# Kernel tuning notes

Measured on AMD Instinct MI355X. Metric: run time of the kernel, lower is better.

Reference implementation:

```python
import jax, jax.numpy as jnp
import numpy as np

ALPHA = 0.95
TH_MIN = 0.4
TH_MAX = 1.5
LN_EPS = 1e-5
NORM_EPS = 1e-12


def setup_inputs() -> dict:
    key = jax.random.key(0)
    ks = jax.random.split(key, 8)
    B, L, H, V = 64, 2048, 128, 32000
    s = 1.0 / np.sqrt(H)
    return {
        "seq": jax.random.randint(ks[0], (B, L), 0, V),
        "embed": jax.random.normal(ks[1], (V, H), jnp.float32),
        "w1": jax.random.normal(ks[2], (H, 2 * H), jnp.float32) * s,
        "b1": jnp.zeros((2 * H,), jnp.float32),
        "w2": jax.random.normal(ks[3], (2 * H, H), jnp.float32) * (1.0 / np.sqrt(2 * H)),
        "b2": jnp.zeros((H,), jnp.float32),
        "ln_g": jnp.ones((H,), jnp.float32),
        "ln_b": jnp.zeros((H,), jnp.float32),
        "kp_w": jax.random.normal(ks[4], (H, H), jnp.float32) * s,
        "rp_w": jax.random.normal(ks[5], (H, H), jnp.float32) * s,
        "rp_b": jnp.zeros((H,), jnp.float32),
        "out_w": jax.random.normal(ks[6], (H, V), jnp.float32) * s,
        "out_b": jnp.zeros((V,), jnp.float32),
    }


def reference(seq, embed, w1, b1, w2, b2, ln_g, ln_b, kp_w, rp_w, rp_b, out_w, out_b):
    # Embedding + residual FFN + LayerNorm
    h = embed[seq]  # [B,L,H]
    x = h + (jnp.maximum(h @ w1 + b1, 0.0) @ w2 + b2)
    mu = jnp.mean(x, axis=-1, keepdims=True)
    var = jnp.mean(jnp.square(x - mu), axis=-1, keepdims=True)
    hn = (x - mu) * jax.lax.rsqrt(var + LN_EPS) * ln_g + ln_b
    B, L, H = hn.shape

    keys = hn @ kp_w  # [B,L,H] all projected keys (kp has no bias)
    ks_t = jnp.swapaxes(keys[:, :-1, :], 0, 1)  # [L-1,B,H] time-major for scan
    t_idx = jnp.arange(L - 1, dtype=hn.dtype)
    thresh = TH_MIN + (TH_MAX - TH_MIN) * (1.0 - t_idx / max(L - 1, 1))  # [L-1]

    def step(M, inputs):
        k, th = inputs  # k: [B,H], th: scalar
        kn = k / jnp.maximum(jnp.linalg.norm(k, axis=-1, keepdims=True), NORM_EPS)
        vp = jnp.einsum('bij,bj->bi', M, kn)  # predicted value
        err = k - vp
        fire = (jnp.linalg.norm(err, axis=-1) >= th * jnp.linalg.norm(k, axis=-1)).astype(M.dtype)
        delta = fire[:, None, None] * (err[:, :, None] * kn[:, None, :])  # gated outer product
        return M + (1.0 - ALPHA) * delta, None

    M0 = jnp.zeros((B, H, H), hn.dtype)
    M, _ = jax.lax.scan(step, M0, (ks_t, thresh))

    q = keys[:, -1, :]
    read = jnp.einsum('bij,bj->bi', M, q)
    return (read @ rp_w + rp_b) @ out_w + out_b
```

## Files before the change

kernel.cpp:

```cpp
#include <hip/hip_runtime.h>

#define HD 128
#define LD 2048
#define BD 64
#define VD 32000
#define NSTEP 2047

#define C_ALPHA  0.05f
#define C_THMIN  0.4f
#define C_THSPAN 1.1f
#define C_NEPS   1e-12f
#define C_LNEPS  1e-5f

#define HSP 132
#define W1P 68
#define W2P 132
#define ATP 68
#define TOK0 896
#define TBLK 9

extern "C" __global__ __launch_bounds__(256, 1)
void k_tokens(const int* __restrict__ seq, const float* __restrict__ embed,
              const float* __restrict__ w1, const float* __restrict__ b1,
              const float* __restrict__ w2, const float* __restrict__ b2,
              const float* __restrict__ lng, const float* __restrict__ lnb,
              const float* __restrict__ kp, float* __restrict__ keys)
{
  extern __shared__ float sm[];
  float* hs = sm;
  float* wt = sm + 128*HSP;
  float* at = wt + 128*W1P;
  const int tid = threadIdx.x;
  const int bb  = blockIdx.x / TBLK;
  const int rel = blockIdx.x % TBLK;
  const long long tokBase = (long long)bb * LD + TOK0 + rel * 128;

  for (int u = tid; u < 128*32; u += 256) {
    const int tok = u >> 5, seg = u & 31;
    const int s = seq[tokBase + tok];
    *(float4*)(hs + tok*HSP + seg*4) =
        *(const float4*)(embed + (long long)s*HD + seg*4);
  }
  __syncthreads();

  const int tg = tid >> 4;
  const int ig = tid & 15;

  float xacc[8][8] = {};

  for (int jt = 0; jt < 4; ++jt) {
    for (int u = tid; u < 128*16; u += 256) {
      const int i = u >> 4, q = u & 15;
      *(float4*)(wt + i*W1P + q*4) =
          *(const float4*)(w1 + (long long)i*256 + jt*64 + q*4);
    }
    __syncthreads();
    {
      float aa[8][4];
      float b1v[4];
      #pragma unroll
      for (int c = 0; c < 4; ++c) b1v[c] = b1[jt*64 + ig*4 + c];
      #pragma unroll
      for (int r = 0; r < 8; ++r)
        #pragma unroll
        for (int c = 0; c < 4; ++c) aa[r][c] = b1v[c];
      #pragma unroll 4
      for (int i4 = 0; i4 < 32; ++i4) {
        float wc[4][4];
        #pragma unroll
        for (int d = 0; d < 4; ++d) {
          float4 u = *(const float4*)(wt + (i4*4 + d)*W1P + ig*4);
          wc[d][0] = u.x; wc[d][1] = u.y; wc[d][2] = u.z; wc[d][3] = u.w;
        }
        #pragma unroll
        for (int r = 0; r < 8; ++r) {
          float4 hv = *(const float4*)(hs + (tg + 16*r)*HSP + i4*4);
          #pragma unroll
          for (int c = 0; c < 4; ++c) {
            aa[r][c] = fmaf(hv.x, wc[0][c], aa[r][c]);
            aa[r][c] = fmaf(hv.y, wc[1][c], aa[r][c]);
            aa[r][c] = fmaf(hv.z, wc[2][c], aa[r][c]);
            aa[r][c] = fmaf(hv.w, wc[3][c], aa[r][c]);
          }
        }
      }
      #pragma unroll
      for (int r = 0; r < 8; ++r) {
        float4 o;
        o.x = fmaxf(aa[r][0], 0.0f); o.y = fmaxf(aa[r][1], 0.0f);
        o.z = fmaxf(aa[r][2], 0.0f); o.w = fmaxf(aa[r][3], 0.0f);
        *(float4*)(at + (tg + 16*r)*ATP + ig*4) = o;
      }
    }
    __syncthreads();
    for (int u = tid; u < 64*32; u += 256) {
      const int k = u >> 5, q = u & 31;
      *(float4*)(wt + k*W2P + q*4) =
          *(const float4*)(w2 + (long long)(jt*64 + k)*128 + q*4);
    }
    __syncthreads();
    #pragma unroll 2
    for (int k4 = 0; k4 < 16; ++k4) {
      float wr[4][8];
      #pragma unroll
      for (int d = 0; d < 4; ++d) {
        float4 u0 = *(const float4*)(wt + (k4*4 + d)*W2P + ig*8);
        float4 u1 = *(const float4*)(wt + (k4*4 + d)*W2P + ig*8 + 4);
        wr[d][0]=u0.x; wr[d][1]=u0.y; wr[d][2]=u0.z; wr[d][3]=u0.w;
        wr[d][4]=u1.x; wr[d][5]=u1.y; wr[d][6]=u1.z; wr[d][7]=u1.w;
      }
      #pragma unroll
      for (int r = 0; r < 8; ++r) {
        float4 av = *(const float4*)(at + (tg + 16*r)*ATP + k4*4);
        #pragma unroll
        for (int cc = 0; cc < 8; ++cc) {
          xacc[r][cc] = fmaf(av.x, wr[0][cc], xacc[r][cc]);
          xacc[r][cc] = fmaf(av.y, wr[1][cc], xacc[r][cc]);
          xacc[r][cc] = fmaf(av.z, wr[2][cc], xacc[r][cc]);
          xacc[r][cc] = fmaf(av.w, wr[3][cc], xacc[r][cc]);
        }
      }
    }
    __syncthreads();
  }

  {
    float b2v[8], gv[8], bv[8];
    #pragma unroll
    for (int cc = 0; cc < 8; ++cc) {
      b2v[cc] = b2[ig*8 + cc]; gv[cc] = lng[ig*8 + cc]; bv[cc] = lnb[ig*8 + cc];
    }
    #pragma unroll
    for (int r = 0; r < 8; ++r) {
      const int row = (tg + 16*r)*HSP + ig*8;
      float4 h0 = *(const float4*)(hs + row);
      float4 h1 = *(const float4*)(hs + row + 4);
      float xr[8];
      xr[0] = h0.x + (xacc[r][0] + b2v[0]);
      xr[1] = h0.y + (xacc[r][1] + b2v[1]);
      xr[2] = h0.z + (xacc[r][2] + b2v[2]);
      xr[3] = h0.w + (xacc[r][3] + b2v[3]);
      xr[4] = h1.x + (xacc[r][4] + b2v[4]);
      xr[5] = h1.y + (xacc[r][5] + b2v[5]);
      xr[6] = h1.z + (xacc[r][6] + b2v[6]);
      xr[7] = h1.w + (xacc[r][7] + b2v[7]);
      float s = xr[0]+xr[1]+xr[2]+xr[3]+xr[4]+xr[5]+xr[6]+xr[7];
      s += __shfl_xor(s, 1, 16); s += __shfl_xor(s, 2, 16);
      s += __shfl_xor(s, 4, 16); s += __shfl_xor(s, 8, 16);
      const float mu = s * 0.0078125f;
      float vs = 0.0f;
      #pragma unroll
      for (int cc = 0; cc < 8; ++cc) { float d = xr[cc]-mu; vs = fmaf(d, d, vs); }
      vs += __shfl_xor(vs, 1, 16); vs += __shfl_xor(vs, 2, 16);
      vs += __shfl_xor(vs, 4, 16); vs += __shfl_xor(vs, 8, 16);
      const float rstd = 1.0f / sqrtf(vs * 0.0078125f + C_LNEPS);
      float4 o0, o1;
      o0.x = (xr[0]-mu)*rstd*gv[0] + bv[0];
      o0.y = (xr[1]-mu)*rstd*gv[1] + bv[1];
      o0.z = (xr[2]-mu)*rstd*gv[2] + bv[2];
      o0.w = (xr[3]-mu)*rstd*gv[3] + bv[3];
      o1.x = (xr[4]-mu)*rstd*gv[4] + bv[4];
      o1.y = (xr[5]-mu)*rstd*gv[5] + bv[5];
      o1.z = (xr[6]-mu)*rstd*gv[6] + bv[6];
      o1.w = (xr[7]-mu)*rstd*gv[7] + bv[7];
      *(float4*)(hs + row) = o0;
      *(float4*)(hs + row + 4) = o1;
    }
  }
  __syncthreads();

  {
    float ky[8][8] = {};
    for (int kt = 0; kt < 2; ++kt) {
      for (int u = tid; u < 64*32; u += 256) {
        const int k = u >> 5, q = u & 31;
        *(float4*)(wt + k*W2P + q*4) =
            *(const float4*)(kp + (long long)(kt*64 + k)*128 + q*4);
      }
      __syncthreads();
      #pragma unroll 2
      for (int k4 = 0; k4 < 16; ++k4) {
        float wr[4][8];
        #pragma unroll
        for (int d = 0; d < 4; ++d) {
          float4 u0 = *(const float4*)(wt + (k4*4 + d)*W2P + ig*8);
          float4 u1 = *(const float4*)(wt + (k4*4 + d)*W2P + ig*8 + 4);
          wr[d][0]=u0.x; wr[d][1]=u0.y; wr[d][2]=u0.z; wr[d][3]=u0.w;
          wr[d][4]=u1.x; wr[d][5]=u1.y; wr[d][6]=u1.z; wr[d][7]=u1.w;
        }
        #pragma unroll
        for (int r = 0; r < 8; ++r) {
          float4 hv = *(const float4*)(hs + (tg + 16*r)*HSP + kt*64 + k4*4);
          #pragma unroll
          for (int cc = 0; cc < 8; ++cc) {
            ky[r][cc] = fmaf(hv.x, wr[0][cc], ky[r][cc]);
            ky[r][cc] = fmaf(hv.y, wr[1][cc], ky[r][cc]);
            ky[r][cc] = fmaf(hv.z, wr[2][cc], ky[r][cc]);
            ky[r][cc] = fmaf(hv.w, wr[3][cc], ky[r][cc]);
          }
        }
      }
      __syncthreads();
    }
    #pragma unroll
    for (int r = 0; r < 8; ++r) {
      const long long g = tokBase + tg + 16*r;
      float4 o0, o1;
      o0.x = ky[r][0]; o0.y = ky[r][1]; o0.z = ky[r][2]; o0.w = ky[r][3];
      o1.x = ky[r][4]; o1.y = ky[r][5]; o1.z = ky[r][6]; o1.w = ky[r][7];
      *(float4*)(keys + g*HD + ig*8) = o0;
      *(float4*)(keys + g*HD + ig*8 + 4) = o1;
    }
  }
}

#define C0 29
#define MSP 132
#define GPW 36
#define NT 768

#define INVB(buf,tok) Gxl[(tok)*GPW + 32 + (buf)]
#define TN2B(buf,tok) Gxl[(tok)*GPW + 34 + (buf)]

__device__ __forceinline__ float dpp_add_b1(float x){int y=__builtin_amdgcn_update_dpp(0,__float_as_int(x),0xB1,0xf,0xf,true);return x+__int_as_float(y);}
__device__ __forceinline__ float dpp_add_4e(float x){int y=__builtin_amdgcn_update_dpp(0,__float_as_int(x),0x4E,0xf,0xf,true);return x+__int_as_float(y);}
__device__ __forceinline__ float dpp_add_hm(float x){int y=__builtin_amdgcn_update_dpp(0,__float_as_int(x),0x141,0xf,0xf,true);return x+__int_as_float(y);}
__device__ __forceinline__ float dpp_add_mr(float x){int y=__builtin_amdgcn_update_dpp(0,__float_as_int(x),0x140,0xf,0xf,true);return x+__int_as_float(y);}
__device__ __forceinline__ float dpp_add_b15(float x){int y=__builtin_amdgcn_update_dpp(0,__float_as_int(x),0x142,0xf,0xf,true);return x+__int_as_float(y);}
__device__ __forceinline__ float dpp_add_b31(float x){int y=__builtin_amdgcn_update_dpp(0,__float_as_int(x),0x143,0xf,0xf,true);return x+__int_as_float(y);}

__device__ __forceinline__ void gram_half(const float* bufS, const float* bufT,
                                          float* dst, int half, int lane)
{
  const int sq = lane & 7, tq = lane >> 3;
  float ga[4][2] = {};
  for (int j4 = 0; j4 < 32; ++j4) {
    const int col = ((j4 + lane) & 31) * 4;
    float4 sv[4], tv[2];
    #pragma unroll
    for (int r = 0; r < 4; ++r)
      sv[r] = *(const float4*)(bufS + (sq + 8*r)*128 + col);
    #pragma unroll
    for (int q = 0; q < 2; ++q)
      tv[q] = *(const float4*)(bufT + (half*16 + tq*2 + q)*128 + col);
    #pragma unroll
    for (int r = 0; r < 4; ++r)
      #pragma unroll
      for (int q = 0; q < 2; ++q) {
        ga[r][q] = fmaf(sv[r].x, tv[q].x, ga[r][q]);
        ga[r][q] = fmaf(sv[r].y, tv[q].y, ga[r][q]);
        ga[r][q] = fmaf(sv[r].z, tv[q].z, ga[r][q]);
        ga[r][q] = fmaf(sv[r].w, tv[q].w, ga[r][q]);
      }
  }
  #pragma unroll
  for (int r = 0; r < 4; ++r)
    #pragma unroll
    for (int q = 0; q < 2; ++q)
      dst[(sq + 8*r)*GPW + half*16 + tq*2 + q] = ga[r][q];
}

extern "C" __global__ __launch_bounds__(768)
void k_scan(const float* __restrict__ keys, float* __restrict__ Mg)
{
  extern __shared__ float sm[];
  float* Msh  = sm;
  float* kbuf = Msh + 128*MSP;
  float* PW   = kbuf + 3*4096;
  float* Gb   = PW + 2*4096;
  float* Gxl  = Gb + 2*32*GPW;

  const int tid  = threadIdx.x;
  const int lane = tid & 63;
  const int w    = tid >> 6;
  const int b    = blockIdx.x;
  const float* kb = keys + (long long)b * LD * HD;

  for (int u = tid; u < 128*MSP; u += NT) Msh[u] = 0.0f;
  for (int u = tid; u < 4096; u += NT) PW[(C0&1)*4096 + u] = 0.0f;
  {
    const int b30 = C0 % 3;
    for (int u = tid; u < 1024; u += NT)
      *(float4*)(kbuf + b30*4096 + u*4) =
          *(const float4*)(kb + (long long)(C0*32)*HD + u*4);
  }
  __syncthreads();
  {
    const float* kc = kbuf + (C0%3)*4096;
    for (int u = tid; u < 1024; u += NT) {
      const int s = u >> 5, t = u & 31;
      float a = 0.0f;
      for (int j4 = 0; j4 < 32; ++j4) {
        const int col = ((j4 + tid) & 31) * 4;
        float4 sv = *(const float4*)(kc + s*128 + col);
        float4 tv = *(const float4*)(kc + t*128 + col);
        a = fmaf(sv.x,tv.x,a); a = fmaf(sv.y,tv.y,a);
        a = fmaf(sv.z,tv.z,a); a = fmaf(sv.w,tv.w,a);
      }
      Gb[(C0&1)*32*GPW + s*GPW + t] = a;
    }
  }
  if (tid < 256) {
    const int tok = tid >> 3, pp = tid & 7;
    const float* kc = kbuf + (C0%3)*4096;
    float ss = 0.0f;
    #pragma unroll
    for (int q = 0; q < 4; ++q) {
      float4 v = *(const float4*)(kc + tok*128 + pp*16 + q*4);
      ss = fmaf(v.x,v.x,ss); ss = fmaf(v.y,v.y,ss);
      ss = fmaf(v.z,v.z,ss); ss = fmaf(v.w,v.w,ss);
    }
    ss += __shfl_xor(ss,1,8); ss += __shfl_xor(ss,2,8); ss += __shfl_xor(ss,4,8);
    if (pp == 0) {
      const float n = sqrtf(ss);
      INVB(C0&1, tok) = 1.0f / fmaxf(n, C_NEPS);
      const float th = C_THMIN + C_THSPAN * (1.0f - (float)(C0*32 + tok) / 2047.0f);
      const float tn = th * n;
      TN2B(C0&1, tok) = tn * tn;
    }
  }
  __syncthreads();

  for (int c = C0; c <= 64; ++c) {
    const int cur = c & 1, nxt = cur ^ 1;
    const int b3c = c % 3;
    const int b3n = (c + 1) % 3;
    const int b3p = (c + 2) % 3;
    const int t0 = c * 32;

    if (w < 8) {
      if (c > C0) {
        const int it = tid >> 5;
        const int jt = tid & 31;
        const int i0 = it*8, j0 = jt*4;
        const float* Wp  = PW + nxt*4096;
        const float* kfp = kbuf + b3p*4096;
        float acc[8][4] = {};
        for (int s = 0; s < 32; ++s) {
          const float4 wa = *(const float4*)(Wp + s*128 + i0);
          const float4 wb = *(const float4*)(Wp + s*128 + i0 + 4);
          const float4 k4 = *(const float4*)(kfp + s*128 + j0);
          float wv[8] = {wa.x,wa.y,wa.z,wa.w,wb.x,wb.y,wb.z,wb.w};
          float kv[4] = {k4.x,k4.y,k4.z,k4.w};
          #pragma unroll
          for (int a = 0; a < 8; ++a)
            #pragma unroll
            for (int q = 0; q < 4; ++q)
              acc[a][q] = fmaf(wv[a], kv[q], acc[a][q]);
        }
        #pragma unroll
        for (int a = 0; a < 8; ++a) {
          float* mp = Msh + (i0 + a)*MSP + j0;
          float4 m = *(float4*)mp;
          m.x = fmaf(C_ALPHA, acc[a][0], m.x);
          m.y = fmaf(C_ALPHA, acc[a][1], m.y);
          m.z = fmaf(C_ALPHA, acc[a][2], m.z);
          m.w = fmaf(C_ALPHA, acc[a][3], m.w);
          *(float4*)mp = m;
        }
      }
    } else {
      const int t2id = tid - 512;
      float4 kvl[4];
      if (c < 63) {
        #pragma unroll
        for (int q = 0; q < 4; ++q)
          kvl[q] = *(const float4*)(kb + (long long)(t0 + 32)*HD + (t2id + 256*q)*4);
      }
      if (c > C0 && c <= 63) {
        const int tt = t2id >> 5;
        const int i0 = (t2id & 31) * 4;
        const int tb4 = tt*4;
        const float* Wp = PW + nxt*4096;
        float fac[4][4] = {};
        for (int s = 0; s < 32; ++s) {
          const float4 gx = *(const float4*)(Gxl + s*GPW + tb4);
          const float4 wp = *(const float4*)(Wp + s*128 + i0);
          float gv[4] = {gx.x,gx.y,gx.z,gx.w};
          float pv[4] = {wp.x,wp.y,wp.z,wp.w};
          #pragma unroll
          for (int a = 0; a < 4; ++a)
            #pragma unroll
            for (int q = 0; q < 4; ++q)
              fac[a][q] = fmaf(gv[a], pv[q], fac[a][q]);
        }
        float* Pp = PW + cur*4096;
        #pragma unroll
        for (int a = 0; a < 4; ++a) {
          float* pp = Pp + (tb4 + a)*128 + i0;
          float4 p = *(float4*)pp;
          p.x = fmaf(C_ALPHA, fac[a][0], p.x);
          p.y = fmaf(C_ALPHA, fac[a][1], p.y);
          p.z = fmaf(C_ALPHA, fac[a][2], p.z);
          p.w = fmaf(C_ALPHA, fac[a][3], p.w);
          *(float4*)pp = p;
        }
      }
      if (c < 63) {
        #pragma unroll
        for (int q = 0; q < 4; ++q)
          *(float4*)(kbuf + b3n*4096 + (t2id + 256*q)*4) = kvl[q];
      }
    }
    __syncthreads();
    if (c == 64) break;

    if (w == 0) {
      float* Pc = PW + cur*4096;
      const float* kfc = kbuf + b3c*4096;
      const float* Gc  = Gb + cur*32*GPW;
      const int l2 = lane*2;
      float2 acc[16];
      #pragma unroll
      for (int u = 0; u < 16; ++u) { acc[u].x = 0.0f; acc[u].y = 0.0f; }
      #pragma unroll
      for (int t = 0; t < 16; ++t) {
        const float2 p2 = *(const float2*)(Pc + t*128 + l2);
        const float2 k2 = *(const float2*)(kfc + t*128 + l2);
        const float it = INVB(cur, t);
        const float vx = it * fmaf(C_ALPHA, acc[t].x, p2.x);
        const float vy = it * fmaf(C_ALPHA, acc[t].y, p2.y);
        const float ex = k2.x - vx;
        const float ey = k2.y - vy;
        float e2 = fmaf(ex, ex, ey*ey);
        e2 = dpp_add_b1(e2); e2 = dpp_add_4e(e2);
        e2 = dpp_add_hm(e2); e2 = dpp_add_mr(e2);
        e2 = dpp_add_b15(e2); e2 = dpp_add_b31(e2);
        const float en2 = __int_as_float(__builtin_amdgcn_readlane(__float_as_int(e2), 63));
        const bool fire = (en2 >= TN2B(cur, t));
        const float wx = fire ? ex * it : 0.0f;
        const float wy = fire ? ey * it : 0.0f;
        float2 w2v; w2v.x = wx; w2v.y = wy;
        *(float2*)(Pc + t*128 + l2) = w2v;
        const float* gr = Gc + t*GPW;
        #pragma unroll
        for (int u4 = (t+1) & ~3; u4 < 16; u4 += 4) {
          const float4 g = *(const float4*)(gr + u4);
          acc[u4+0].x = fmaf(wx, g.x, acc[u4+0].x); acc[u4+0].y = fmaf(wy, g.x, acc[u4+0].y);
          acc[u4+1].x = fmaf(wx, g.y, acc[u4+1].x); acc[u4+1].y = fmaf(wy, g.y, acc[u4+1].y);
          acc[u4+2].x = fmaf(wx, g.z, acc[u4+2].x); acc[u4+2].y = fmaf(wy, g.z, acc[u4+2].y);
          acc[u4+3].x = fmaf(wx, g.w, acc[u4+3].x); acc[u4+3].y = fmaf(wy, g.w, acc[u4+3].y);
        }
      }
      #pragma unroll
      for (int u = 0; u < 16; ++u) { acc[u].x = 0.0f; acc[u].y = 0.0f; }
      #pragma unroll
      for (int s = 0; s < 16; ++s) {
        const float2 ws = *(const float2*)(Pc + s*128 + l2);
        const float* gs = Gc + s*GPW + 16;
        #pragma unroll
        for (int u4 = 0; u4 < 16; u4 += 4) {
          const float4 g = *(const float4*)(gs + u4);
          acc[u4+0].x = fmaf(ws.x, g.x, acc[u4+0].x); acc[u4+0].y = fmaf(ws.y, g.x, acc[u4+0].y);
          acc[u4+1].x = fmaf(ws.x, g.y, acc[u4+1].x); acc[u4+1].y = fmaf(ws.y, g.y, acc[u4+1].y);
          acc[u4+2].x = fmaf(ws.x, g.z, acc[u4+2].x); acc[u4+2].y = fmaf(ws.y, g.z, acc[u4+2].y);
          acc[u4+3].x = fmaf(ws.x, g.w, acc[u4+3].x); acc[u4+3].y = fmaf(ws.y, g.w, acc[u4+3].y);
        }
      }
      #pragma unroll
      for (int t = 16; t < 32; ++t) {
        const int tt = t - 16;
        const float2 p2 = *(const float2*)(Pc + t*128 + l2);
        const float2 k2 = *(const float2*)(kfc + t*128 + l2);
        const float it = INVB(cur, t);
        const float vx = it * fmaf(C_ALPHA, acc[tt].x, p2.x);
        const float vy = it * fmaf(C_ALPHA, acc[tt].y, p2.y);
        const float ex = k2.x - vx;
        const float ey = k2.y - vy;
        float e2 = fmaf(ex, ex, ey*ey);
        e2 = dpp_add_b1(e2); e2 = dpp_add_4e(e2);
        e2 = dpp_add_hm(e2); e2 = dpp_add_mr(e2);
        e2 = dpp_add_b15(e2); e2 = dpp_add_b31(e2);
        const float en2 = __int_as_float(__builtin_amdgcn_readlane(__float_as_int(e2), 63));
        const bool fire = (en2 >= TN2B(cur, t)) && (t0 + t < NSTEP);
        const float wx = fire ? ex * it : 0.0f;
        const float wy = fire ? ey * it : 0.0f;
        float2 w2v; w2v.x = wx; w2v.y = wy;
        *(float2*)(Pc + t*128 + l2) = w2v;
        const float* gr = Gc + t*GPW + 16;
        #pragma unroll
        for (int u4 = (tt+1) & ~3; u4 < 16; u4 += 4) {
          const float4 g = *(const float4*)(gr + u4);
          acc[u4+0].x = fmaf(wx, g.x, acc[u4+0].x); acc[u4+0].y = fmaf(wy, g.x, acc[u4+0].y);
          acc[u4+1].x = fmaf(wx, g.y, acc[u4+1].x); acc[u4+1].y = fmaf(wy, g.y, acc[u4+1].y);
          acc[u4+2].x = fmaf(wx, g.z, acc[u4+2].x); acc[u4+2].y = fmaf(wy, g.z, acc[u4+2].y);
          acc[u4+3].x = fmaf(wx, g.w, acc[u4+3].x); acc[u4+3].y = fmaf(wy, g.w, acc[u4+3].y);
        }
      }
    } else if (c < 63) {
      int p;
      switch (w) {
        case 4:  p = 0; break;  case 8:  p = 1; break;
        case 1:  p = 2; break;  case 5:  p = 3; break;  case 9:  p = 4; break;
        case 2:  p = 5; break;  case 6:  p = 6; break;  case 10: p = 7; break;
        default: p = -1;
      }
      if (p >= 0) {
        const float* kfn = kbuf + b3n*4096;
        const int tb4 = p*4;
        const int ib = lane & 31, ih = lane >> 5;
        float pa[4][2] = {};
        for (int j4 = 0; j4 < 32; ++j4) {
          float4 kv[4], mv[2];
          #pragma unroll
          for (int ss = 0; ss < 4; ++ss)
            kv[ss] = *(const float4*)(kfn + (tb4+ss)*128 + j4*4);
          #pragma unroll
          for (int r = 0; r < 2; ++r)
            mv[r] = *(const float4*)(Msh + (ib + 32*(ih + 2*r))*MSP + j4*4);
          #pragma unroll
          for (int ss = 0; ss < 4; ++ss)
            #pragma unroll
            for (int r = 0; r < 2; ++r) {
              pa[ss][r] = fmaf(kv[ss].x, mv[r].x, pa[ss][r]);
              pa[ss][r] = fmaf(kv[ss].y, mv[r].y, pa[ss][r]);
              pa[ss][r] = fmaf(kv[ss].z, mv[r].z, pa[ss][r]);
              pa[ss][r] = fmaf(kv[ss].w, mv[r].w, pa[ss][r]);
            }
        }
        float* Pp = PW + nxt*4096;
        #pragma unroll
        for (int ss = 0; ss < 4; ++ss)
          #pragma unroll
          for (int r = 0; r < 2; ++r)
            Pp[(tb4+ss)*128 + ib + 32*(ih + 2*r)] = pa[ss][r];
        if (w == 4) {
          const float* kn = kbuf + b3n*4096;
          const int tok = lane >> 1, hh = lane & 1;
          float ss2 = 0.0f;
          #pragma unroll
          for (int q = 0; q < 16; ++q) {
            const int cq = (q + lane) & 15;
            float4 v = *(const float4*)(kn + tok*128 + hh*64 + cq*4);
            ss2 = fmaf(v.x,v.x,ss2); ss2 = fmaf(v.y,v.y,ss2);
            ss2 = fmaf(v.z,v.z,ss2); ss2 = fmaf(v.w,v.w,ss2);
          }
          ss2 += __shfl_xor(ss2, 1);
          if (hh == 0) {
            const float n = sqrtf(ss2);
            INVB(nxt, tok) = 1.0f / fmaxf(n, C_NEPS);
            const float th = C_THMIN + C_THSPAN * (1.0f - (float)(t0 + 32 + tok) / 2047.0f);
            const float tn = th * n;
            TN2B(nxt, tok) = tn * tn;
          }
        }
      } else if (w == 3) {
        gram_half(kbuf + b3n*4096, kbuf + b3n*4096, Gb + nxt*32*GPW, 0, lane);
      } else if (w == 7) {
        gram_half(kbuf + b3n*4096, kbuf + b3n*4096, Gb + nxt*32*GPW, 1, lane);
      } else {
        gram_half(kbuf + b3c*4096, kbuf + b3n*4096, Gxl, 0, lane);
        gram_half(kbuf + b3c*4096, kbuf + b3n*4096, Gxl, 1, lane);
      }
    }
    __syncthreads();
  }

  for (int u = tid; u < 4096; u += NT) {
    const int i = u >> 5, q = u & 31;
    *(float4*)(Mg + (long long)b*16384 + i*128 + q*4) =
        *(const float4*)(Msh + i*MSP + q*4);
  }
}

extern "C" __global__ __launch_bounds__(128, 1)
void k_read(const float* __restrict__ keys, const float* __restrict__ Mg,
            const float* __restrict__ rpw, const float* __restrict__ rpb,
            float* __restrict__ rr)
{
  __shared__ float qv[128];
  __shared__ float rd[128];
  const int b = blockIdx.x, tid = threadIdx.x;
  qv[tid] = keys[((long long)b*LD + (LD-1))*HD + tid];
  __syncthreads();
  float acc = 0.0f;
  const float* Mrow = Mg + (long long)b*16384 + (long long)tid*128;
  for (int j4 = 0; j4 < 32; ++j4) {
    float4 m = *(const float4*)(Mrow + j4*4);
    acc = fmaf(m.x, qv[j4*4+0], acc);
    acc = fmaf(m.y, qv[j4*4+1], acc);
    acc = fmaf(m.z, qv[j4*4+2], acc);
    acc = fmaf(m.w, qv[j4*4+3], acc);
  }
  rd[tid] = acc;
  __syncthreads();
  float a2 = rpb[tid];
  for (int k = 0; k < 128; ++k) a2 = fmaf(rd[k], rpw[k*128 + tid], a2);
  rr[b*128 + tid] = a2;
}

extern "C" __global__ __launch_bounds__(256, 1)
void k_out(const float* __restrict__ rr, const float* __restrict__ outw,
           const float* __restrict__ outb, float* __restrict__ out)
{
  __shared__ float rl[64*128];
  const int tid = threadIdx.x;
  for (int u = tid; u < 8192; u += 256) rl[u] = rr[u];
  __syncthreads();
  const int v = blockIdx.x*128 + (tid & 127);
  const int bg = tid >> 7;
  const float ob = outb[v];
  float acc[32];
  #pragma unroll
  for (int bb = 0; bb < 32; ++bb) acc[bb] = 0.0f;
  for (int h = 0; h < 128; ++h) {
    const float wv = outw[(long long)h*VD + v];
    #pragma unroll
    for (int bb = 0; bb < 32; ++bb)
      acc[bb] = fmaf(rl[(bg*32 + bb)*128 + h], wv, acc[bb]);
  }
  #pragma unroll
  for (int bb = 0; bb < 32; ++bb)
    out[(long long)(bg*32 + bb)*VD + v] = acc[bb] + ob;
}

extern "C" void kernel_launch(void* const* d_in, const int* in_sizes, int n_in,
                              void* d_out, int out_size, void* d_ws, size_t ws_size,
                              hipStream_t stream)
{
  const int*   seq   = (const int*)d_in[0];
  const float* embed = (const float*)d_in[1];
  const float* w1    = (const float*)d_in[2];
  const float* b1    = (const float*)d_in[3];
  const float* w2    = (const float*)d_in[4];
  const float* b2    = (const float*)d_in[5];
  const float* ln_g  = (const float*)d_in[6];
  const float* ln_b  = (const float*)d_in[7];
  const float* kp_w  = (const float*)d_in[8];
  const float* rp_w  = (const float*)d_in[9];
  const float* rp_b  = (const float*)d_in[10];
  const float* out_w = (const float*)d_in[11];
  const float* out_b = (const float*)d_in[12];
  float* out = (float*)d_out;

  char* ws = (char*)d_ws;
  float* keys = (float*)ws;
  float* Mg   = (float*)(ws + 67108864);
  float* rr   = (float*)(ws + 67108864 + 4194304);

  hipLaunchKernelGGL(k_tokens, dim3(64*TBLK), dim3(256), 137216, stream,
                     seq, embed, w1, b1, w2, b2, ln_g, ln_b, kp_w, keys);
  hipLaunchKernelGGL(k_scan, dim3(64), dim3(768), 163328, stream, keys, Mg);
  hipLaunchKernelGGL(k_read, dim3(64), dim3(128), 0, stream, keys, Mg, rp_w, rp_b, rr);
  hipLaunchKernelGGL(k_out, dim3(250), dim3(256), 0, stream, rr, out_w, out_b, out);
}
```

Before: 780.2 us.

## Shrink scan block to 512 threads and redistribute per-chunk work across 8 waves

Reduces the k_scan workgroup from 12 to 8 wavefronts and rebalances the chunk work among them. The M update and the P-factor update now run on all 8 waves instead of separate wave groups. The projection, Gram and norm tasks are reassigned: waves 1-4 each handle 8 tokens, waves 5-7 handle quarter-Gram pieces, and wave 7 also computes the norms. Fewer waves should cut barrier cost and per-wave overhead, but with only 64 blocks there is less parallelism to hide LDS latency, and each wave carries more serial work.

```diff
diff --git a/kernel.cpp b/kernel.cpp
--- a/kernel.cpp
+++ b/kernel.cpp
@@ -217,7 +217,7 @@
 #define C0 29
 #define MSP 132
 #define GPW 36
-#define NT 768
+#define NT 512
 
 #define INVB(buf,tok) Gxl[(tok)*GPW + 32 + (buf)]
 #define TN2B(buf,tok) Gxl[(tok)*GPW + 34 + (buf)]
@@ -229,38 +229,28 @@
 __device__ __forceinline__ float dpp_add_b15(float x){int y=__builtin_amdgcn_update_dpp(0,__float_as_int(x),0x142,0xf,0xf,true);return x+__int_as_float(y);}
 __device__ __forceinline__ float dpp_add_b31(float x){int y=__builtin_amdgcn_update_dpp(0,__float_as_int(x),0x143,0xf,0xf,true);return x+__int_as_float(y);}
 
-__device__ __forceinline__ void gram_half(const float* bufS, const float* bufT,
-                                          float* dst, int half, int lane)
+__device__ __forceinline__ void gram_q(const float* bufS, const float* bufT,
+                                       float* dst, int q, int lane)
 {
   const int sq = lane & 7, tq = lane >> 3;
-  float ga[4][2] = {};
+  const int tcol = q*8 + tq;
+  float ga[4] = {};
   for (int j4 = 0; j4 < 32; ++j4) {
     const int col = ((j4 + lane) & 31) * 4;
-    float4 sv[4], tv[2];
+    const float4 tv = *(const float4*)(bufT + tcol*128 + col);
     #pragma unroll
-    for (int r = 0; r < 4; ++r)
-      sv[r] = *(const float4*)(bufS + (sq + 8*r)*128 + col);
-    #pragma unroll
-    for (int q = 0; q < 2; ++q)
-      tv[q] = *(const float4*)(bufT + (half*16 + tq*2 + q)*128 + col);
-    #pragma unroll
-    for (int r = 0; r < 4; ++r)
-      #pragma unroll
-      for (int q = 0; q < 2; ++q) {
-        ga[r][q] = fmaf(sv[r].x, tv[q].x, ga[r][q]);
-        ga[r][q] = fmaf(sv[r].y, tv[q].y, ga[r][q]);
-        ga[r][q] = fmaf(sv[r].z, tv[q].z, ga[r][q]);
-        ga[r][q] = fmaf(sv[r].w, tv[q].w, ga[r][q]);
-      }
+    for (int r = 0; r < 4; ++r) {
+      const float4 sv = *(const float4*)(bufS + (sq + 8*r)*128 + col);
+      ga[r] = fmaf(sv.x, tv.x, ga[r]); ga[r] = fmaf(sv.y, tv.y, ga[r]);
+      ga[r] = fmaf(sv.z, tv.z, ga[r]); ga[r] = fmaf(sv.w, tv.w, ga[r]);
+    }
   }
   #pragma unroll
   for (int r = 0; r < 4; ++r)
-    #pragma unroll
-    for (int q = 0; q < 2; ++q)
-      dst[(sq + 8*r)*GPW + half*16 + tq*2 + q] = ga[r][q];
+    dst[(sq + 8*r)*GPW + tcol] = ga[r];
 }
 
-extern "C" __global__ __launch_bounds__(768)
+extern "C" __global__ __launch_bounds__(512)
 void k_scan(const float* __restrict__ keys, float* __restrict__ Mg)
 {
   extern __shared__ float sm[];
@@ -328,8 +318,14 @@
     const int b3p = (c + 2) % 3;
     const int t0 = c * 32;
 
-    if (w < 8) {
-      if (c > C0) {
+    float4 kvl0, kvl1;
+    if (c < 63) {
+      const float* src = kb + (long long)(t0 + 32)*HD;
+      kvl0 = *(const float4*)(src + tid*4);
+      kvl1 = *(const float4*)(src + (tid + 512)*4);
+    }
+    if (c > C0) {
+      {
         const int it = tid >> 5;
         const int jt = tid & 31;
         const int i0 = it*8, j0 = jt*4;
@@ -359,35 +355,27 @@
           *(float4*)mp = m;
         }
       }
-    } else {
-      const int t2id = tid - 512;
-      float4 kvl[4];
-      if (c < 63) {
-        #pragma unroll
-        for (int q = 0; q < 4; ++q)
-          kvl[q] = *(const float4*)(kb + (long long)(t0 + 32)*HD + (t2id + 256*q)*4);
-      }
-      if (c > C0 && c <= 63) {
-        const int tt = t2id >> 5;
-        const int i0 = (t2id & 31) * 4;
-        const int tb4 = tt*4;
+      if (c <= 63) {
+        const int tt2 = tid >> 5;
+        const int i0f = (tid & 31) * 4;
         const float* Wp = PW + nxt*4096;
-        float fac[4][4] = {};
+        float fac[2][4] = {};
         for (int s = 0; s < 32; ++s) {
-          const float4 gx = *(const float4*)(Gxl + s*GPW + tb4);
-          const float4 wp = *(const float4*)(Wp + s*128 + i0);
-          float gv[4] = {gx.x,gx.y,gx.z,gx.w};
-          float pv[4] = {wp.x,wp.y,wp.z,wp.w};
-          #pragma unroll
-          for (int a = 0; a < 4; ++a)
-            #pragma unroll
-            for (int q = 0; q < 4; ++q)
-              fac[a][q] = fmaf(gv[a], pv[q], fac[a][q]);
+          const float2 gx = *(const float2*)(Gxl + s*GPW + tt2*2);
+          const float4 wp = *(const float4*)(Wp + s*128 + i0f);
+          fac[0][0] = fmaf(gx.x, wp.x, fac[0][0]);
+          fac[0][1] = fmaf(gx.x, wp.y, fac[0][1]);
+          fac[0][2] = fmaf(gx.x, wp.z, fac[0][2]);
+          fac[0][3] = fmaf(gx.x, wp.w, fac[0][3]);
+          fac[1][0] = fmaf(gx.y, wp.x, fac[1][0]);
+          fac[1][1] = fmaf(gx.y, wp.y, fac[1][1]);
+          fac[1][2] = fmaf(gx.y, wp.z, fac[1][2]);
+          fac[1][3] = fmaf(gx.y, wp.w, fac[1][3]);
         }
         float* Pp = PW + cur*4096;
         #pragma unroll
-        for (int a = 0; a < 4; ++a) {
-          float* pp = Pp + (tb4 + a)*128 + i0;
+        for (int a = 0; a < 2; ++a) {
+          float* pp = Pp + (tt2*2 + a)*128 + i0f;
           float4 p = *(float4*)pp;
           p.x = fmaf(C_ALPHA, fac[a][0], p.x);
           p.y = fmaf(C_ALPHA, fac[a][1], p.y);
@@ -396,11 +384,11 @@
           *(float4*)pp = p;
         }
       }
-      if (c < 63) {
-        #pragma unroll
-        for (int q = 0; q < 4; ++q)
-          *(float4*)(kbuf + b3n*4096 + (t2id + 256*q)*4) = kvl[q];
-      }
+    }
+    if (c < 63) {
+      float* dst = kbuf + b3n*4096;
+      *(float4*)(dst + tid*4) = kvl0;
+      *(float4*)(dst + (tid + 512)*4) = kvl1;
     }
     __syncthreads();
     if (c == 64) break;
@@ -488,69 +476,64 @@
         }
       }
     } else if (c < 63) {
-      int p;
-      switch (w) {
-        case 4:  p = 0; break;  case 8:  p = 1; break;
-        case 1:  p = 2; break;  case 5:  p = 3; break;  case 9:  p = 4; break;
-        case 2:  p = 5; break;  case 6:  p = 6; break;  case 10: p = 7; break;
-        default: p = -1;
-      }
-      if (p >= 0) {
+      if (w <= 4) {
         const float* kfn = kbuf + b3n*4096;
-        const int tb4 = p*4;
+        const int tb8 = (w - 1) * 8;
         const int ib = lane & 31, ih = lane >> 5;
-        float pa[4][2] = {};
+        float pa[8][2] = {};
         for (int j4 = 0; j4 < 32; ++j4) {
-          float4 kv[4], mv[2];
-          #pragma unroll
-          for (int ss = 0; ss < 4; ++ss)
-            kv[ss] = *(const float4*)(kfn + (tb4+ss)*128 + j4*4);
+          float4 mv[2];
           #pragma unroll
           for (int r = 0; r < 2; ++r)
             mv[r] = *(const float4*)(Msh + (ib + 32*(ih + 2*r))*MSP + j4*4);
           #pragma unroll
-          for (int ss = 0; ss < 4; ++ss)
-            #pragma unroll
-            for (int r = 0; r < 2; ++r) {
-              pa[ss][r] = fmaf(kv[ss].x, mv[r].x, pa[ss][r]);
-              pa[ss][r] = fmaf(kv[ss].y, mv[r].y, pa[ss][r]);
-              pa[ss][r] = fmaf(kv[ss].z, mv[r].z, pa[ss][r]);
-              pa[ss][r] = fmaf(kv[ss].w, mv[r].w, pa[ss][r]);
-            }
+          for (int ss = 0; ss < 8; ++ss) {
+            const float4 kv = *(const float4*)(kfn + (tb8+ss)*128 + j4*4);
+            pa[ss][0] = fmaf(kv.x, mv[0].x, pa[ss][0]);
+            pa[ss][0] = fmaf(kv.y, mv[0].y, pa[ss][0]);
+            pa[ss][0] = fmaf(kv.z, mv[0].z, pa[ss][0]);
+            pa[ss][0] = fmaf(kv.w, mv[0].w, pa[ss][0]);
+            pa[ss][1] = fmaf(kv.x, mv[1].x, pa[ss][1]);
+            pa[ss][1] = fmaf(kv.y, mv[1].y, pa[ss][1]);
+            pa[ss][1] = fmaf(kv.z, mv[1].z, pa[ss][1]);
+            pa[ss][1] = fmaf(kv.w, mv[1].w, pa[ss][1]);
+          }
         }
         float* Pp = PW + nxt*4096;
         #pragma unroll
-        for (int ss = 0; ss < 4; ++ss)
+        for (int ss = 0; ss < 8; ++ss)
           #pragma unroll
           for (int r = 0; r < 2; ++r)
-            Pp[(tb4+ss)*128 + ib + 32*(ih + 2*r)] = pa[ss][r];
-        if (w == 4) {
-          const float* kn = kbuf + b3n*4096;
-          const int tok = lane >> 1, hh = lane & 1;
-          float ss2 = 0.0f;
-          #pragma unroll
-          for (int q = 0; q < 16; ++q) {
-            const int cq = (q + lane) & 15;
-            float4 v = *(const float4*)(kn + tok*128 + hh*64 + cq*4);
-            ss2 = fmaf(v.x,v.x,ss2); ss2 = fmaf(v.y,v.y,ss2);
-            ss2 = fmaf(v.z,v.z,ss2); ss2 = fmaf(v.w,v.w,ss2);
-          }
-          ss2 += __shfl_xor(ss2, 1);
-          if (hh == 0) {
-            const float n = sqrtf(ss2);
-            INVB(nxt, tok) = 1.0f / fmaxf(n, C_NEPS);
-            const float th = C_THMIN + C_THSPAN * (1.0f - (float)(t0 + 32 + tok) / 2047.0f);
-            const float tn = th * n;
-            TN2B(nxt, tok) = tn * tn;
-          }
-        }
-      } else if (w == 3) {
-        gram_half(kbuf + b3n*4096, kbuf + b3n*4096, Gb + nxt*32*GPW, 0, lane);
-      } else if (w == 7) {
-        gram_half(kbuf + b3n*4096, kbuf + b3n*4096, Gb + nxt*32*GPW, 1, lane);
+            Pp[(tb8+ss)*128 + ib + 32*(ih + 2*r)] = pa[ss][r];
+      } else if (w == 5) {
+        gram_q(kbuf + b3n*4096, kbuf + b3n*4096, Gb + nxt*32*GPW, 0, lane);
+        gram_q(kbuf + b3n*4096, kbuf + b3n*4096, Gb + nxt*32*GPW, 1, lane);
+        gram_q(kbuf + b3n*4096, kbuf + b3n*4096, Gb + nxt*32*GPW, 2, lane);
+      } else if (w == 6) {
+        gram_q(kbuf + b3n*4096, kbuf + b3n*4096, Gb + nxt*32*GPW, 3, lane);
+        gram_q(kbuf + b3c*4096, kbuf + b3n*4096, Gxl, 0, lane);
+        gram_q(kbuf + b3c*4096, kbuf + b3n*4096, Gxl, 1, lane);
       } else {
-        gram_half(kbuf + b3c*4096, kbuf + b3n*4096, Gxl, 0, lane);
-        gram_half(kbuf + b3c*4096, kbuf + b3n*4096, Gxl, 1, lane);
+        gram_q(kbuf + b3c*4096, kbuf + b3n*4096, Gxl, 2, lane);
+        gram_q(kbuf + b3c*4096, kbuf + b3n*4096, Gxl, 3, lane);
+        const float* kn = kbuf + b3n*4096;
+        const int tok = lane >> 1, hh = lane & 1;
+        float ss2 = 0.0f;
+        #pragma unroll
+        for (int q = 0; q < 16; ++q) {
+          const int cq = (q + lane) & 15;
+          float4 v = *(const float4*)(kn + tok*128 + hh*64 + cq*4);
+          ss2 = fmaf(v.x,v.x,ss2); ss2 = fmaf(v.y,v.y,ss2);
+          ss2 = fmaf(v.z,v.z,ss2); ss2 = fmaf(v.w,v.w,ss2);
+        }
+        ss2 += __shfl_xor(ss2, 1);
+        if (hh == 0) {
+          const float n = sqrtf(ss2);
+          INVB(nxt, tok) = 1.0f / fmaxf(n, C_NEPS);
+          const float th = C_THMIN + C_THSPAN * (1.0f - (float)(t0 + 32 + tok) / 2047.0f);
+          const float tn = th * n;
+          TN2B(nxt, tok) = tn * tn;
+        }
       }
     }
     __syncthreads();
@@ -640,7 +623,7 @@
 
   hipLaunchKernelGGL(k_tokens, dim3(64*TBLK), dim3(256), 137216, stream,
                      seq, embed, w1, b1, w2, b2, ln_g, ln_b, kp_w, keys);
-  hipLaunchKernelGGL(k_scan, dim3(64), dim3(768), 163328, stream, keys, Mg);
+  hipLaunchKernelGGL(k_scan, dim3(64), dim3(512), 163328, stream, keys, Mg);
   hipLaunchKernelGGL(k_read, dim3(64), dim3(128), 0, stream, keys, Mg, rp_w, rp_b, rr);
   hipLaunchKernelGGL(k_out, dim3(250), dim3(256), 0, stream, rr, out_w, out_b, out);
 }
```

Result: slower. 969.7 us (+24.3%).
